# Optimization experiments

Measured on AMD Instinct MI355X. Metric: run time of the kernel, lower is better.

The kernel has to match this reference:

```python
import jax, jax.numpy as jnp
import numpy as np

FISTA_ITER = 50
LAMBDA = 0.1
POWER_ITER = 100


def power_method(W):
    # Estimates c = largest eigenvalue of W^T W (squared spectral norm).
    # Torch code uses a random init vector; we use a fixed key for determinism.
    X0 = jax.random.normal(jax.random.key(1), (1, W.shape[1]), dtype=W.dtype)

    def body(i, carry):
        X, _ = carry
        X = (X @ W.T) @ W            # [1, m]
        nm = jnp.linalg.norm(X)
        return (X / nm, nm)

    _, nm = jax.lax.fori_loop(0, POWER_ITER, body, (X0, jnp.asarray(1.0, W.dtype)))
    return nm


def soft_threshold(X, lam):
    return jnp.sign(X) * jax.nn.relu(jnp.abs(X) - lam)


def fista(Y, W, lam, iters):
    c = power_method(W)
    eta = 1.0 / c
    Gamma0 = soft_threshold(Y @ (eta * W), lam)   # [B, m]
    Y_norm = jnp.linalg.norm(Y)
    t0 = jnp.asarray(1.0, Y.dtype)

    def step(carry, _):
        Gamma, Z, t = carry
        residual = Z @ W.T - Y                                   # [B, n]
        Gamma_new = soft_threshold(Z - eta * (residual @ W), lam / c)
        t_new = (1.0 + jnp.sqrt(1.0 + 4.0 * t ** 2)) / 2.0
        Z_new = Gamma_new + (t - 1.0) / t_new * (Gamma_new - Gamma)
        nrm = jnp.linalg.norm(residual) / Y_norm
        return (Gamma_new, Z_new, t_new), nrm

    (Gamma, _, _), norms = jax.lax.scan(step, (Gamma0, Gamma0, t0), None, length=iters)
    return Gamma, norms


def setup_inputs() -> dict:
    key = jax.random.key(0)
    k1, k2 = jax.random.split(key)
    Y = jax.random.normal(k1, (8192, 784), dtype=jnp.float32)
    W = jax.random.normal(k2, (784, 2048), dtype=jnp.float32)
    W = W / jnp.linalg.norm(W, axis=0, keepdims=True)  # NormDict
    return {"Y": Y, "W": W}


def reference(Y, W):
    Gamma, norms = fista(Y, W, LAMBDA, FISTA_ITER)
    X = Gamma @ W.T                  # reconstruction [B, 784]
    return (X, Gamma, norms)
```

## Files before the change

kernel.cpp:

```cpp
#include <hip/hip_runtime.h>
#include <math.h>

#define B_DIM   8192
#define N_DIM   784
#define NPAD    800
#define NROWS_W 896
#define M_DIM   2048
#define XSZ     (B_DIM*N_DIM)
#define GSZ     (B_DIM*M_DIM)
#define NITER   50
#define PITER   100

typedef __attribute__((ext_vector_type(8))) short short8;
typedef __attribute__((ext_vector_type(4))) float floatx4;

__device__ __forceinline__ void async_ld16(const unsigned short* g, unsigned short* l){
  __builtin_amdgcn_global_load_lds(
      (const __attribute__((address_space(1))) unsigned int*)g,
      (__attribute__((address_space(3))) unsigned int*)l,
      16, 0, 0);
}

__device__ __forceinline__ unsigned rotl32(unsigned x, int d){ return (x<<d)|(x>>(32-d)); }

__device__ void threefry2x32(unsigned& v0, unsigned& v1){
  const unsigned ks0=0u, ks1=1u, ks2=0x1BD11BDBu;
  unsigned x0=v0+ks0, x1=v1+ks1;
#define RND(R) { x0+=x1; x1=rotl32(x1,R); x1^=x0; }
  RND(13) RND(15) RND(26) RND(6)
  x0+=ks1; x1+=ks2+1u;
  RND(17) RND(29) RND(16) RND(24)
  x0+=ks2; x1+=ks0+2u;
  RND(13) RND(15) RND(26) RND(6)
  x0+=ks0; x1+=ks1+3u;
  RND(17) RND(29) RND(16) RND(24)
  x0+=ks1; x1+=ks2+4u;
  RND(13) RND(15) RND(26) RND(6)
  x0+=ks2; x1+=ks0+5u;
#undef RND
  v0=x0; v1=x1;
}

__device__ float erfinv_f(float x){
  float w = -logf((1.0f-x)*(1.0f+x));
  float p;
  if (w < 5.0f){
    w -= 2.5f;
    p = 2.81022636e-08f;
    p = fmaf(p,w, 3.43273939e-07f);
    p = fmaf(p,w,-3.5233877e-06f);
    p = fmaf(p,w,-4.39150654e-06f);
    p = fmaf(p,w, 0.00021858087f);
    p = fmaf(p,w,-0.00125372503f);
    p = fmaf(p,w,-0.00417768164f);
    p = fmaf(p,w, 0.246640727f);
    p = fmaf(p,w, 1.50140941f);
  } else {
    w = sqrtf(w) - 3.0f;
    p = -0.000200214257f;
    p = fmaf(p,w, 0.000100950558f);
    p = fmaf(p,w, 0.00134934322f);
    p = fmaf(p,w,-0.00367342844f);
    p = fmaf(p,w, 0.00573950773f);
    p = fmaf(p,w,-0.0076224613f);
    p = fmaf(p,w, 0.00943887047f);
    p = fmaf(p,w, 1.00167406f);
    p = fmaf(p,w, 2.83297682f);
  }
  return p*x;
}

__device__ float bits_to_normal(unsigned b){
  unsigned fb = (b>>9) | 0x3f800000u;
  float u01 = __uint_as_float(fb) - 1.0f;
  const float lo = -0.99999994f;
  float u = u01*(1.0f - lo) + lo;
  u = fmaxf(lo, u);
  return 1.41421356237f * erfinv_f(u);
}

__global__ void setup_kernel(float* __restrict__ xbuf0, float* __restrict__ accs){
  int i = threadIdx.x;
  if (i < 64) accs[i] = 0.0f;
  unsigned v0 = (unsigned)i, v1 = (unsigned)(1024+i);
  threefry2x32(v0, v1);
  xbuf0[i]        = bits_to_normal(v0);
  xbuf0[1024 + i] = bits_to_normal(v1);
}

__device__ __forceinline__ unsigned short f2bf(float f){
  unsigned u = __float_as_uint(f);
  unsigned r = (u + 0x7fffu + ((u>>16)&1u)) >> 16;
  return (unsigned short)r;
}
__device__ __forceinline__ unsigned pack2(float a, float b){
  return (unsigned)f2bf(a) | ((unsigned)f2bf(b) << 16);
}
__device__ __forceinline__ float bf2f(unsigned short s){
  return __uint_as_float(((unsigned)s) << 16);
}

__global__ void conv_w(const float* __restrict__ W, unsigned short* __restrict__ Wbf){
  int i4 = (blockIdx.x*256 + threadIdx.x)*4;
  int row = i4 >> 11;
  uint2 p = make_uint2(0,0);
  if (row < N_DIM){
    float4 v = *(const float4*)(W + (size_t)row*M_DIM + (i4 & 2047));
    p.x = pack2(v.x, v.y); p.y = pack2(v.z, v.w);
  }
  *(uint2*)(Wbf + i4) = p;
}

__global__ void conv_y(const float* __restrict__ Y, unsigned short* __restrict__ Ybf){
  int row = blockIdx.x;
  int c4 = threadIdx.x*4;
  if (c4 >= NPAD) return;
  uint2 p = make_uint2(0,0);
  if (c4 < N_DIM){
    float4 v = *(const float4*)(Y + (size_t)row*N_DIM + c4);
    p.x = pack2(v.x, v.y); p.y = pack2(v.z, v.w);
  }
  *(uint2*)(Ybf + (size_t)row*NPAD + c4) = p;
}

__global__ void transpose_w(const float* __restrict__ W, unsigned short* __restrict__ WTbf){
  __shared__ float tile[32][33];
  int k0 = blockIdx.x*32;
  int j0 = blockIdx.y*32;
  int tx = threadIdx.x & 31, ty = threadIdx.x >> 5;
#pragma unroll
  for (int i=0;i<4;i++){
    int j = j0 + ty + 8*i;
    float v = (j < N_DIM) ? W[(size_t)j*M_DIM + k0 + tx] : 0.0f;
    tile[tx][ty+8*i] = v;
  }
  __syncthreads();
#pragma unroll
  for (int i=0;i<4;i++){
    int k = k0 + ty + 8*i;
    WTbf[(size_t)k*NPAD + j0 + tx] = f2bf(tile[ty+8*i][tx]);
  }
}

__global__ __launch_bounds__(256)
void compute_q(const float* __restrict__ W, float* __restrict__ Q){
  __shared__ float As2[16][132];
  __shared__ float Bs2[16][132];
  const int t = threadIdx.x;
  const int a0 = blockIdx.x*128, b0 = blockIdx.y*128;
  const int ty = t>>4, tx = t&15;
  float acc[8][8];
#pragma unroll
  for (int i=0;i<8;i++)
#pragma unroll
    for (int j=0;j<8;j++) acc[i][j]=0.0f;

  for (int j0=0; j0<N_DIM; j0+=16){
#pragma unroll
    for (int h=0; h<8; ++h){
      int idx = h*256 + t;
      int r = idx>>7, c = idx&127;
      As2[r][c] = W[(size_t)(j0+r)*M_DIM + a0 + c];
      Bs2[r][c] = W[(size_t)(j0+r)*M_DIM + b0 + c];
    }
    __syncthreads();
#pragma unroll
    for (int kk=0; kk<16; ++kk){
      float a[8], b[8];
#pragma unroll
      for (int i=0;i<8;i++) a[i] = As2[kk][ty*8+i];
#pragma unroll
      for (int j=0;j<8;j++) b[j] = Bs2[kk][tx*8+j];
#pragma unroll
      for (int i=0;i<8;i++)
#pragma unroll
        for (int j=0;j<8;j++) acc[i][j] = fmaf(a[i], b[j], acc[i][j]);
    }
    __syncthreads();
  }
#pragma unroll
  for (int i=0;i<8;i++){
    int a = a0 + ty*8 + i;
#pragma unroll
    for (int j=0;j<8;j++) Q[(size_t)a*M_DIM + b0 + tx*8 + j] = acc[i][j];
  }
}

__global__ void sumsq_kernel(const float* __restrict__ v, int n, float* __restrict__ acc){
  __shared__ float red[256];
  int t = threadIdx.x;
  float s = 0.0f;
  for (int i = blockIdx.x*256 + t; i < n; i += gridDim.x*256){ float x = v[i]; s = fmaf(x,x,s); }
  red[t] = s; __syncthreads();
  for (int off=128; off>0; off>>=1){ if (t<off) red[t]+=red[t+off]; __syncthreads(); }
  if (t==0) atomicAdd(acc, red[0]);
}

__global__ void pm_q(const float* __restrict__ x, const float* __restrict__ Q,
                     float* __restrict__ xout){
  __shared__ float red[256];
  int t = threadIdx.x;
  float s = 0.0f;
  for (int k=t; k<M_DIM; k+=256){ float v = x[k]; s = fmaf(v,v,s); }
  red[t]=s; __syncthreads();
  for (int off=128; off>0; off>>=1){ if (t<off) red[t]+=red[t+off]; __syncthreads(); }
  float inv = 1.0f/sqrtf(red[0]);
  int wave = t>>6, lane = t&63;
  int j = blockIdx.x*4 + wave;
  const float* Qr = Q + (size_t)j*M_DIM;
  float acc = 0.0f;
  for (int k=lane; k<M_DIM; k+=64) acc = fmaf(x[k], Qr[k], acc);
  for (int off=32; off>0; off>>=1) acc += __shfl_down(acc, off);
  if (lane==0) xout[j] = acc * inv;
}

__global__ void finish_power(const float* __restrict__ xfin, const float* __restrict__ accs,
                             float* __restrict__ params){
  __shared__ float red[256];
  int t = threadIdx.x;
  float s = 0.0f;
  for (int k=t; k<M_DIM; k+=256){ float v = xfin[k]; s = fmaf(v,v,s); }
  red[t]=s; __syncthreads();
  for (int off=128; off>0; off>>=1){ if (t<off) red[t]+=red[t+off]; __syncthreads(); }
  if (t==0){
    float c = sqrtf(red[0]);
    params[0] = c;
    params[1] = 1.0f/c;
    params[2] = 0.1f/c;
    params[3] = sqrtf(accs[0]);
  }
}

__device__ __forceinline__ float softthr(float v, float th){
  float a = fmaxf(fabsf(v) - th, 0.0f);
  return copysignf(a, v);
}

template<int MODE>
__global__ __launch_bounds__(256)
void mfma_nt(const unsigned short* __restrict__ Abf,
             const unsigned short* __restrict__ Bbf,
             const float* __restrict__ Wf,
             const float* __restrict__ Y,
             unsigned short* __restrict__ Rbf,
             float* __restrict__ X,
             float* __restrict__ nacc){
  __shared__ float4 smem4[1024];
  unsigned short* As = (unsigned short*)smem4;
  unsigned short* Bs = As + 64*32;
  float* fbuf = (float*)smem4;

  const int t    = threadIdx.x;
  const int m0   = blockIdx.x*64, n0 = blockIdx.y*128;
  const int wave = t>>6, lane = t&63;
  const int wm2  = wave>>1, wn2 = wave&1;
  const int quad = lane>>4, l15 = lane&15;
  const int lrow = lane>>2;
  const int lk   = (lane&3)*8;
  const int sr   = t>>1;
  const int skq  = (t&1)*16;

  floatx4 acc[2][4];
#pragma unroll
  for (int i=0;i<2;i++)
#pragma unroll
    for (int j=0;j<4;j++) acc[i][j] = (floatx4)(0.0f);

  for (int k0=0; k0<M_DIM; k0+=32){
    async_ld16(Abf + (size_t)(m0 + wave*16 + lrow)*M_DIM + k0 + lk, &As[wave*512]);
    if (MODE==0){
#pragma unroll
      for (int c=0; c<2; ++c){
        int chunk = wave*2 + c;
        async_ld16(Bbf + (size_t)(n0 + chunk*16 + lrow)*M_DIM + k0 + lk, &Bs[chunk*512]);
      }
    } else {
      int j = n0 + sr;
      uint4 p0 = make_uint4(0,0,0,0), p1 = make_uint4(0,0,0,0);
      if (j < N_DIM){
        const float* bp = Wf + (size_t)j*M_DIM + k0 + skq;
        float4 v0 = *(const float4*)(bp+0);
        float4 v1 = *(const float4*)(bp+4);
        float4 v2 = *(const float4*)(bp+8);
        float4 v3 = *(const float4*)(bp+12);
        p0.x=pack2(v0.x,v0.y); p0.y=pack2(v0.z,v0.w); p0.z=pack2(v1.x,v1.y); p0.w=pack2(v1.z,v1.w);
        p1.x=pack2(v2.x,v2.y); p1.y=pack2(v2.z,v2.w); p1.z=pack2(v3.x,v3.y); p1.w=pack2(v3.z,v3.w);
      }
      *(uint4*)&Bs[sr*32 + skq]     = p0;
      *(uint4*)&Bs[sr*32 + skq + 8] = p1;
    }
    __syncthreads();
    short8 af[2], bfr[4];
#pragma unroll
    for (int ti=0; ti<2; ++ti)
      af[ti] = *(const short8*)&As[(wm2*32 + ti*16 + l15)*32 + quad*8];
#pragma unroll
    for (int tj=0; tj<4; ++tj)
      bfr[tj] = *(const short8*)&Bs[(wn2*64 + tj*16 + l15)*32 + quad*8];
#pragma unroll
    for (int ti=0; ti<2; ++ti)
#pragma unroll
      for (int tj=0; tj<4; ++tj)
        acc[ti][tj] = __builtin_amdgcn_mfma_f32_16x16x32_bf16(af[ti], bfr[tj], acc[ti][tj], 0, 0, 0);
    __syncthreads();
  }

  float ss = 0.0f;
#pragma unroll
  for (int c=0; c<2; ++c){
    if (wn2 == c){
#pragma unroll
      for (int ti=0; ti<2; ++ti)
#pragma unroll
        for (int tj=0; tj<4; ++tj)
#pragma unroll
          for (int r=0; r<4; ++r)
            fbuf[(wm2*32 + ti*16 + quad*4 + r)*64 + tj*16 + l15] = acc[ti][tj][r];
    }
    __syncthreads();
#pragma unroll
    for (int k=0; k<4; ++k){
      int row = k*16 + (t>>4);
      int col = (t&15)*4;
      int m = m0 + row;
      int n = n0 + c*64 + col;
      float4 v = *(const float4*)&fbuf[row*64 + col];
      if (MODE==0){
        if (n < N_DIM){
          float4 yv = *(const float4*)(Y + (size_t)m*N_DIM + n);
          float r0 = v.x - yv.x, r1 = v.y - yv.y, r2 = v.z - yv.z, r3 = v.w - yv.w;
          uint2 p; p.x = pack2(r0, r1); p.y = pack2(r2, r3);
          *(uint2*)(Rbf + (size_t)m*NPAD + n) = p;
          ss = fmaf(r0,r0, fmaf(r1,r1, fmaf(r2,r2, fmaf(r3,r3, ss))));
        } else if (n < NPAD){
          *(uint2*)(Rbf + (size_t)m*NPAD + n) = make_uint2(0,0);
        }
      } else {
        if (n < N_DIM) *(float4*)(X + (size_t)m*N_DIM + n) = v;
      }
    }
    __syncthreads();
  }

  if (MODE==0){
    for (int off=32; off>0; off>>=1) ss += __shfl_down(ss, off);
    if (lane==0) atomicAdd(nacc, ss);
  }
}

template<int MODE>
__global__ __launch_bounds__(256)
void mfma_nn(const unsigned short* __restrict__ Abf,
             const unsigned short* __restrict__ WTbf,
             float* __restrict__ Gamma,
             unsigned short* __restrict__ Zhi,
             unsigned short* __restrict__ Zlo,
             const float* __restrict__ params,
             float mu){
  __shared__ float4 smem4[1024];
  unsigned short* As = (unsigned short*)smem4;
  unsigned short* Bs = As + 128*32;
  float* fbuf = (float*)smem4;

  const int t    = threadIdx.x;
  const int m0   = blockIdx.x*128, n0 = blockIdx.y*128;
  const int wave = t>>6, lane = t&63;
  const int wm   = wave>>1, wn = wave&1;
  const int quad = lane>>4, l15 = lane&15;
  const int ch0  = wave*2;
  const int lrow = lane>>2;
  const int lk   = (lane&3)*8;

  floatx4 acc[4][4];
#pragma unroll
  for (int i=0;i<4;i++)
#pragma unroll
    for (int j=0;j<4;j++) acc[i][j] = (floatx4)(0.0f);

  for (int k0=0; k0<NPAD; k0+=32){
#pragma unroll
    for (int c=0; c<2; ++c){
      int chunk = ch0 + c;
      async_ld16(Abf  + (size_t)(m0 + chunk*16 + lrow)*NPAD + k0 + lk, &As[chunk*512]);
      async_ld16(WTbf + (size_t)(n0 + chunk*16 + lrow)*NPAD + k0 + lk, &Bs[chunk*512]);
    }
    __syncthreads();
    short8 af[4], bfr[4];
#pragma unroll
    for (int ti=0; ti<4; ++ti)
      af[ti] = *(const short8*)&As[(wm*64 + ti*16 + l15)*32 + quad*8];
#pragma unroll
    for (int tj=0; tj<4; ++tj)
      bfr[tj] = *(const short8*)&Bs[(wn*64 + tj*16 + l15)*32 + quad*8];
#pragma unroll
    for (int ti=0; ti<4; ++ti)
#pragma unroll
      for (int tj=0; tj<4; ++tj)
        acc[ti][tj] = __builtin_amdgcn_mfma_f32_16x16x32_bf16(af[ti], bfr[tj], acc[ti][tj], 0, 0, 0);
    __syncthreads();
  }

  const float eta  = params[1];
  const float lamc = params[2];

#pragma unroll
  for (int c=0; c<4; ++c){
    if (wn == (c>>1)){
      int tjb = (c&1)*2;
#pragma unroll
      for (int ti=0; ti<4; ++ti)
#pragma unroll
        for (int u=0; u<2; ++u)
#pragma unroll
          for (int r=0; r<4; ++r)
            fbuf[(wm*64 + ti*16 + quad*4 + r)*32 + u*16 + l15] = acc[ti][tjb+u][r];
    }
    __syncthreads();
#pragma unroll
    for (int k=0; k<4; ++k){
      int row = k*32 + (t>>3);
      int col = (t&7)*4;
      int m = m0 + row;
      int n = n0 + c*32 + col;
      size_t idx = (size_t)m*M_DIM + n;
      float4 g4 = *(const float4*)&fbuf[row*32 + col];
      float gr[4] = {g4.x, g4.y, g4.z, g4.w};
      float go4[4];
      if (MODE!=0){
        uint2 ph = *(const uint2*)(Zhi + idx);
        uint2 pl = *(const uint2*)(Zlo + idx);
        unsigned short h[4] = {(unsigned short)(ph.x&0xffff),(unsigned short)(ph.x>>16),
                               (unsigned short)(ph.y&0xffff),(unsigned short)(ph.y>>16)};
        unsigned short l[4] = {(unsigned short)(pl.x&0xffff),(unsigned short)(pl.x>>16),
                               (unsigned short)(pl.y&0xffff),(unsigned short)(pl.y>>16)};
        float4 gov = *(const float4*)(Gamma + idx);
        go4[0]=gov.x; go4[1]=gov.y; go4[2]=gov.z; go4[3]=gov.w;
#pragma unroll
        for (int e=0;e<4;e++){
          float zv = bf2f(h[e]) + bf2f(l[e]);
          gr[e] = softthr(zv - eta*gr[e], lamc);
        }
      } else {
#pragma unroll
        for (int e=0;e<4;e++) gr[e] = softthr(eta*gr[e], 0.1f);
      }
      *(float4*)(Gamma + idx) = make_float4(gr[0],gr[1],gr[2],gr[3]);
      if (MODE==1){
        float zn[4];
#pragma unroll
        for (int e=0;e<4;e++) zn[e] = gr[e] + mu*(gr[e] - go4[e]);
        unsigned short h0=f2bf(zn[0]), h1=f2bf(zn[1]), h2=f2bf(zn[2]), h3=f2bf(zn[3]);
        uint2 ph; ph.x = (unsigned)h0 | ((unsigned)h1<<16); ph.y = (unsigned)h2 | ((unsigned)h3<<16);
        uint2 pl; pl.x = pack2(zn[0]-bf2f(h0), zn[1]-bf2f(h1));
                  pl.y = pack2(zn[2]-bf2f(h2), zn[3]-bf2f(h3));
        *(uint2*)(Zhi + idx) = ph;
        *(uint2*)(Zlo + idx) = pl;
      } else if (MODE==0){
        unsigned short h0=f2bf(gr[0]), h1=f2bf(gr[1]), h2=f2bf(gr[2]), h3=f2bf(gr[3]);
        uint2 ph; ph.x = (unsigned)h0 | ((unsigned)h1<<16); ph.y = (unsigned)h2 | ((unsigned)h3<<16);
        uint2 pl; pl.x = pack2(gr[0]-bf2f(h0), gr[1]-bf2f(h1));
                  pl.y = pack2(gr[2]-bf2f(h2), gr[3]-bf2f(h3));
        *(uint2*)(Zhi + idx) = ph;
        *(uint2*)(Zlo + idx) = pl;
      } else {
        uint2 ph; ph.x = pack2(gr[0], gr[1]); ph.y = pack2(gr[2], gr[3]);
        *(uint2*)(Zhi + idx) = ph;
      }
    }
    __syncthreads();
  }
}

__global__ void norms_finalize(const float* __restrict__ nacc, const float* __restrict__ params,
                               float* __restrict__ out){
  int i = threadIdx.x;
  if (i < NITER) out[i] = sqrtf(nacc[i]) / params[3];
}

extern "C" void kernel_launch(void* const* d_in, const int* in_sizes, int n_in,
                              void* d_out, int out_size, void* d_ws, size_t ws_size,
                              hipStream_t stream){
  const float* Y  = (const float*)d_in[0];
  const float* W  = (const float*)d_in[1];
  float* out      = (float*)d_out;
  float* X        = out;
  float* Gamma    = out + XSZ;
  float* norms    = out + XSZ + GSZ;

  unsigned short* Zhi = (unsigned short*)d_ws;
  unsigned short* Zlo = Zhi + (size_t)B_DIM*M_DIM;

  unsigned short* Wbf  = (unsigned short*)out;
  unsigned short* WTbf = Wbf + (size_t)NROWS_W*M_DIM;
  unsigned short* Rbf  = WTbf + (size_t)M_DIM*NPAD;
  float* Q      = (float*)Rbf;
  float* fsc    = (float*)(Rbf + (size_t)M_DIM*M_DIM*2);
  float* xb0    = fsc;
  float* xb1    = xb0 + M_DIM;
  float* params = xb1 + M_DIM;
  float* accs   = params + 8;

  setup_kernel<<<dim3(1), dim3(1024), 0, stream>>>(xb0, accs);
  sumsq_kernel<<<dim3(512), dim3(256), 0, stream>>>(Y, XSZ, accs);
  conv_w      <<<dim3(1792), dim3(256), 0, stream>>>(W, Wbf);
  transpose_w <<<dim3(64,25), dim3(256), 0, stream>>>(W, WTbf);

  compute_q<<<dim3(16,16), dim3(256), 0, stream>>>(W, Q);
  float* xa = xb0; float* xc = xb1;
  for (int it=0; it<PITER; ++it){
    pm_q<<<dim3(512), dim3(256), 0, stream>>>(xa, Q, xc);
    float* tmp = xa; xa = xc; xc = tmp;
  }
  finish_power<<<dim3(1), dim3(256), 0, stream>>>(xa, accs, params);

  conv_y<<<dim3(B_DIM), dim3(256), 0, stream>>>(Y, Rbf);

  mfma_nn<0><<<dim3(64,16), dim3(256), 0, stream>>>(Rbf, WTbf, Gamma, Zhi, Zlo, params, 0.0f);

  float tcur = 1.0f;
  for (int it=0; it<NITER; ++it){
    mfma_nt<0><<<dim3(128,7), dim3(256), 0, stream>>>(Zhi, Wbf, nullptr, Y, Rbf, nullptr, accs + 1 + it);
    float tsq = tcur*tcur;
    float tn  = (1.0f + sqrtf(1.0f + 4.0f*tsq)) / 2.0f;
    float mu  = (tcur - 1.0f) / tn;
    tcur = tn;
    if (it < NITER-1)
      mfma_nn<1><<<dim3(64,16), dim3(256), 0, stream>>>(Rbf, WTbf, Gamma, Zhi, Zlo, params, mu);
    else
      mfma_nn<2><<<dim3(64,16), dim3(256), 0, stream>>>(Rbf, WTbf, Gamma, Zhi, Zlo, params, mu);
  }

  norms_finalize<<<dim3(1), dim3(64), 0, stream>>>(accs + 1, params, norms);

  mfma_nt<1><<<dim3(128,7), dim3(256), 0, stream>>>(Zhi, nullptr, W, nullptr, nullptr, X, nullptr);
}
```

Baseline: 9.635 ms.

## Widen GEMM tiles to 256 columns with XCD-aware block mapping

Both MFMA GEMM kernels now compute 256-column output tiles per block (doubling accumulators per wave) and use a 1D grid of 512 blocks whose index is remapped so consecutive blocks land on the same XCD group and share A rows. Scratch buffers (Wbf, WTbf, Rbf, Q) move from the output buffer into the workspace, and the final reconstruction reuses the padded bf16 W copy instead of converting fp32 W inline. This aims to cut redundant operand loads and improve L2 locality, at the cost of higher register pressure, more LDS, and fewer blocks than CUs for wave-level parallelism.

After: 9.278 ms. -3.7%, faster.

```diff
diff --git a/kernel.cpp b/kernel.cpp
--- a/kernel.cpp
+++ b/kernel.cpp
@@ -4,7 +4,7 @@
 #define B_DIM   8192
 #define N_DIM   784
 #define NPAD    800
-#define NROWS_W 896
+#define NROWS_W 1024
 #define M_DIM   2048
 #define XSZ     (B_DIM*N_DIM)
 #define GSZ     (B_DIM*M_DIM)
@@ -240,82 +240,68 @@
 __global__ __launch_bounds__(256)
 void mfma_nt(const unsigned short* __restrict__ Abf,
              const unsigned short* __restrict__ Bbf,
-             const float* __restrict__ Wf,
              const float* __restrict__ Y,
              unsigned short* __restrict__ Rbf,
              float* __restrict__ X,
              float* __restrict__ nacc){
-  __shared__ float4 smem4[1024];
+  __shared__ float4 smem4[1280];
   unsigned short* As = (unsigned short*)smem4;
   unsigned short* Bs = As + 64*32;
   float* fbuf = (float*)smem4;
 
+  const int bid = blockIdx.x;
+  const int g8  = bid & 7, w = bid >> 3;
+  const int m0  = (g8*16 + (w>>2))*64;
+  const int n0  = (w & 3)*256;
+
   const int t    = threadIdx.x;
-  const int m0   = blockIdx.x*64, n0 = blockIdx.y*128;
   const int wave = t>>6, lane = t&63;
   const int wm2  = wave>>1, wn2 = wave&1;
   const int quad = lane>>4, l15 = lane&15;
   const int lrow = lane>>2;
   const int lk   = (lane&3)*8;
-  const int sr   = t>>1;
-  const int skq  = (t&1)*16;
-
-  floatx4 acc[2][4];
+
+  floatx4 acc[2][8];
 #pragma unroll
   for (int i=0;i<2;i++)
 #pragma unroll
-    for (int j=0;j<4;j++) acc[i][j] = (floatx4)(0.0f);
+    for (int j=0;j<8;j++) acc[i][j] = (floatx4)(0.0f);
 
   for (int k0=0; k0<M_DIM; k0+=32){
     async_ld16(Abf + (size_t)(m0 + wave*16 + lrow)*M_DIM + k0 + lk, &As[wave*512]);
-    if (MODE==0){
-#pragma unroll
-      for (int c=0; c<2; ++c){
-        int chunk = wave*2 + c;
-        async_ld16(Bbf + (size_t)(n0 + chunk*16 + lrow)*M_DIM + k0 + lk, &Bs[chunk*512]);
-      }
-    } else {
-      int j = n0 + sr;
-      uint4 p0 = make_uint4(0,0,0,0), p1 = make_uint4(0,0,0,0);
-      if (j < N_DIM){
-        const float* bp = Wf + (size_t)j*M_DIM + k0 + skq;
-        float4 v0 = *(const float4*)(bp+0);
-        float4 v1 = *(const float4*)(bp+4);
-        float4 v2 = *(const float4*)(bp+8);
-        float4 v3 = *(const float4*)(bp+12);
-        p0.x=pack2(v0.x,v0.y); p0.y=pack2(v0.z,v0.w); p0.z=pack2(v1.x,v1.y); p0.w=pack2(v1.z,v1.w);
-        p1.x=pack2(v2.x,v2.y); p1.y=pack2(v2.z,v2.w); p1.z=pack2(v3.x,v3.y); p1.w=pack2(v3.z,v3.w);
-      }
-      *(uint4*)&Bs[sr*32 + skq]     = p0;
-      *(uint4*)&Bs[sr*32 + skq + 8] = p1;
-    }
-    __syncthreads();
-    short8 af[2], bfr[4];
+#pragma unroll
+    for (int c=0; c<4; ++c){
+      int chunk = wave*4 + c;
+      async_ld16(Bbf + (size_t)(n0 + chunk*16 + lrow)*M_DIM + k0 + lk, &Bs[chunk*512]);
+    }
+    __syncthreads();
+    short8 af[2], bfr[8];
 #pragma unroll
     for (int ti=0; ti<2; ++ti)
       af[ti] = *(const short8*)&As[(wm2*32 + ti*16 + l15)*32 + quad*8];
 #pragma unroll
-    for (int tj=0; tj<4; ++tj)
-      bfr[tj] = *(const short8*)&Bs[(wn2*64 + tj*16 + l15)*32 + quad*8];
+    for (int tj=0; tj<8; ++tj)
+      bfr[tj] = *(const short8*)&Bs[(wn2*128 + tj*16 + l15)*32 + quad*8];
 #pragma unroll
     for (int ti=0; ti<2; ++ti)
 #pragma unroll
-      for (int tj=0; tj<4; ++tj)
+      for (int tj=0; tj<8; ++tj)
         acc[ti][tj] = __builtin_amdgcn_mfma_f32_16x16x32_bf16(af[ti], bfr[tj], acc[ti][tj], 0, 0, 0);
     __syncthreads();
   }
 
   float ss = 0.0f;
 #pragma unroll
-  for (int c=0; c<2; ++c){
-    if (wn2 == c){
+  for (int c=0; c<4; ++c){
+    if (wn2 == (c>>1)){
+      int tb = (c&1)*4;
 #pragma unroll
       for (int ti=0; ti<2; ++ti)
 #pragma unroll
-        for (int tj=0; tj<4; ++tj)
+        for (int u=0; u<4; ++u)
 #pragma unroll
           for (int r=0; r<4; ++r)
-            fbuf[(wm2*32 + ti*16 + quad*4 + r)*64 + tj*16 + l15] = acc[ti][tj][r];
+            fbuf[(wm2*32 + ti*16 + quad*4 + r)*64 + u*16 + l15] = acc[ti][tb+u][r];
     }
     __syncthreads();
 #pragma unroll
@@ -357,45 +343,52 @@
              unsigned short* __restrict__ Zlo,
              const float* __restrict__ params,
              float mu){
-  __shared__ float4 smem4[1024];
+  __shared__ float4 smem4[1536];
   unsigned short* As = (unsigned short*)smem4;
   unsigned short* Bs = As + 128*32;
   float* fbuf = (float*)smem4;
 
+  const int bid = blockIdx.x;
+  const int g8  = bid & 7, w = bid >> 3;
+  const int m0  = (g8*8 + (w>>3))*128;
+  const int n0  = (w & 7)*256;
+
   const int t    = threadIdx.x;
-  const int m0   = blockIdx.x*128, n0 = blockIdx.y*128;
   const int wave = t>>6, lane = t&63;
   const int wm   = wave>>1, wn = wave&1;
   const int quad = lane>>4, l15 = lane&15;
-  const int ch0  = wave*2;
   const int lrow = lane>>2;
   const int lk   = (lane&3)*8;
 
-  floatx4 acc[4][4];
+  floatx4 acc[4][8];
 #pragma unroll
   for (int i=0;i<4;i++)
 #pragma unroll
-    for (int j=0;j<4;j++) acc[i][j] = (floatx4)(0.0f);
+    for (int j=0;j<8;j++) acc[i][j] = (floatx4)(0.0f);
 
   for (int k0=0; k0<NPAD; k0+=32){
 #pragma unroll
     for (int c=0; c<2; ++c){
-      int chunk = ch0 + c;
-      async_ld16(Abf  + (size_t)(m0 + chunk*16 + lrow)*NPAD + k0 + lk, &As[chunk*512]);
+      int chunk = wave*2 + c;
+      async_ld16(Abf + (size_t)(m0 + chunk*16 + lrow)*NPAD + k0 + lk, &As[chunk*512]);
+    }
+#pragma unroll
+    for (int c=0; c<4; ++c){
+      int chunk = wave*4 + c;
       async_ld16(WTbf + (size_t)(n0 + chunk*16 + lrow)*NPAD + k0 + lk, &Bs[chunk*512]);
     }
     __syncthreads();
-    short8 af[4], bfr[4];
+    short8 af[4], bfr[8];
 #pragma unroll
     for (int ti=0; ti<4; ++ti)
       af[ti] = *(const short8*)&As[(wm*64 + ti*16 + l15)*32 + quad*8];
 #pragma unroll
-    for (int tj=0; tj<4; ++tj)
-      bfr[tj] = *(const short8*)&Bs[(wn*64 + tj*16 + l15)*32 + quad*8];
+    for (int tj=0; tj<8; ++tj)
+      bfr[tj] = *(const short8*)&Bs[(wn*128 + tj*16 + l15)*32 + quad*8];
 #pragma unroll
     for (int ti=0; ti<4; ++ti)
 #pragma unroll
-      for (int tj=0; tj<4; ++tj)
+      for (int tj=0; tj<8; ++tj)
         acc[ti][tj] = __builtin_amdgcn_mfma_f32_16x16x32_bf16(af[ti], bfr[tj], acc[ti][tj], 0, 0, 0);
     __syncthreads();
   }
@@ -404,16 +397,16 @@
   const float lamc = params[2];
 
 #pragma unroll
-  for (int c=0; c<4; ++c){
-    if (wn == (c>>1)){
-      int tjb = (c&1)*2;
+  for (int c=0; c<8; ++c){
+    if (wn == (c>>2)){
+      int tb = (c&3)*2;
 #pragma unroll
       for (int ti=0; ti<4; ++ti)
 #pragma unroll
         for (int u=0; u<2; ++u)
 #pragma unroll
           for (int r=0; r<4; ++r)
-            fbuf[(wm*64 + ti*16 + quad*4 + r)*32 + u*16 + l15] = acc[ti][tjb+u][r];
+            fbuf[(wm*64 + ti*16 + quad*4 + r)*32 + u*16 + l15] = acc[ti][tb+u][r];
     }
     __syncthreads();
 #pragma unroll
@@ -487,23 +480,22 @@
   float* Gamma    = out + XSZ;
   float* norms    = out + XSZ + GSZ;
 
-  unsigned short* Zhi = (unsigned short*)d_ws;
-  unsigned short* Zlo = Zhi + (size_t)B_DIM*M_DIM;
-
-  unsigned short* Wbf  = (unsigned short*)out;
-  unsigned short* WTbf = Wbf + (size_t)NROWS_W*M_DIM;
-  unsigned short* Rbf  = WTbf + (size_t)M_DIM*NPAD;
-  float* Q      = (float*)Rbf;
-  float* fsc    = (float*)(Rbf + (size_t)M_DIM*M_DIM*2);
-  float* xb0    = fsc;
+  unsigned short* Zhi  = (unsigned short*)d_ws;
+  unsigned short* Zlo  = Zhi  + (size_t)GSZ;
+  unsigned short* Rbf  = Zlo  + (size_t)GSZ;
+  unsigned short* Wbf  = Rbf  + (size_t)B_DIM*NPAD;
+  unsigned short* WTbf = Wbf  + (size_t)NROWS_W*M_DIM;
+  float* Q      = (float*)(WTbf + (size_t)M_DIM*NPAD);
+  float* xb0    = Q + (size_t)M_DIM*M_DIM;
   float* xb1    = xb0 + M_DIM;
   float* params = xb1 + M_DIM;
   float* accs   = params + 8;
 
   setup_kernel<<<dim3(1), dim3(1024), 0, stream>>>(xb0, accs);
   sumsq_kernel<<<dim3(512), dim3(256), 0, stream>>>(Y, XSZ, accs);
-  conv_w      <<<dim3(1792), dim3(256), 0, stream>>>(W, Wbf);
+  conv_w      <<<dim3(2048), dim3(256), 0, stream>>>(W, Wbf);
   transpose_w <<<dim3(64,25), dim3(256), 0, stream>>>(W, WTbf);
+  conv_y      <<<dim3(B_DIM), dim3(256), 0, stream>>>(Y, Rbf);
 
   compute_q<<<dim3(16,16), dim3(256), 0, stream>>>(W, Q);
   float* xa = xb0; float* xc = xb1;
@@ -513,24 +505,22 @@
   }
   finish_power<<<dim3(1), dim3(256), 0, stream>>>(xa, accs, params);
 
-  conv_y<<<dim3(B_DIM), dim3(256), 0, stream>>>(Y, Rbf);
-
-  mfma_nn<0><<<dim3(64,16), dim3(256), 0, stream>>>(Rbf, WTbf, Gamma, Zhi, Zlo, params, 0.0f);
+  mfma_nn<0><<<dim3(512), dim3(256), 0, stream>>>(Rbf, WTbf, Gamma, Zhi, Zlo, params, 0.0f);
 
   float tcur = 1.0f;
   for (int it=0; it<NITER; ++it){
-    mfma_nt<0><<<dim3(128,7), dim3(256), 0, stream>>>(Zhi, Wbf, nullptr, Y, Rbf, nullptr, accs + 1 + it);
+    mfma_nt<0><<<dim3(512), dim3(256), 0, stream>>>(Zhi, Wbf, Y, Rbf, nullptr, accs + 1 + it);
     float tsq = tcur*tcur;
     float tn  = (1.0f + sqrtf(1.0f + 4.0f*tsq)) / 2.0f;
     float mu  = (tcur - 1.0f) / tn;
     tcur = tn;
     if (it < NITER-1)
-      mfma_nn<1><<<dim3(64,16), dim3(256), 0, stream>>>(Rbf, WTbf, Gamma, Zhi, Zlo, params, mu);
+      mfma_nn<1><<<dim3(512), dim3(256), 0, stream>>>(Rbf, WTbf, Gamma, Zhi, Zlo, params, mu);
     else
-      mfma_nn<2><<<dim3(64,16), dim3(256), 0, stream>>>(Rbf, WTbf, Gamma, Zhi, Zlo, params, mu);
+      mfma_nn<2><<<dim3(512), dim3(256), 0, stream>>>(Rbf, WTbf, Gamma, Zhi, Zlo, params, mu);
   }
 
   norms_finalize<<<dim3(1), dim3(64), 0, stream>>>(accs + 1, params, norms);
 
-  mfma_nt<1><<<dim3(128,7), dim3(256), 0, stream>>>(Zhi, nullptr, W, nullptr, nullptr, X, nullptr);
-}
+  mfma_nt<1><<<dim3(512), dim3(256), 0, stream>>>(Zhi, Wbf, nullptr, nullptr, X, nullptr);
+}
```

## Remap GEMM blocks for XCD-aware locality and move scratch buffers to workspace

Applied to the files above, without the earlier changes.

Both MFMA kernels now launch on a 1D grid and remap block ids so that consecutive ids spread across the 8 XCDs (bid&7). Each XCD works on a contiguous band of rows, which should improve L2 reuse of the A and B tiles. Scratch buffers (bf16 W, W^T, residual, Q) move from the output region into the workspace. That lets the final reconstruction GEMM read the prebuilt bf16 W through async loads instead of converting fp32 W on the fly, and conv_y is launched earlier. The approach needs a large enough workspace, and the block-id mapping assumes the XCDs are assigned round-robin.

New measurement: 9.500 ms. Within noise of the previous version (-1.4%).

```diff
diff --git a/kernel.cpp b/kernel.cpp
--- a/kernel.cpp
+++ b/kernel.cpp
@@ -240,7 +240,6 @@
 __global__ __launch_bounds__(256)
 void mfma_nt(const unsigned short* __restrict__ Abf,
              const unsigned short* __restrict__ Bbf,
-             const float* __restrict__ Wf,
              const float* __restrict__ Y,
              unsigned short* __restrict__ Rbf,
              float* __restrict__ X,
@@ -250,15 +249,18 @@
   unsigned short* Bs = As + 64*32;
   float* fbuf = (float*)smem4;
 
+  const int bid = blockIdx.x;
+  const int g8  = bid & 7, w = bid >> 3;
+  const int mt  = w / 7, nt = w - mt*7;
+  const int m0  = (g8*16 + mt)*64;
+  const int n0  = nt*128;
+
   const int t    = threadIdx.x;
-  const int m0   = blockIdx.x*64, n0 = blockIdx.y*128;
   const int wave = t>>6, lane = t&63;
   const int wm2  = wave>>1, wn2 = wave&1;
   const int quad = lane>>4, l15 = lane&15;
   const int lrow = lane>>2;
   const int lk   = (lane&3)*8;
-  const int sr   = t>>1;
-  const int skq  = (t&1)*16;
 
   floatx4 acc[2][4];
 #pragma unroll
@@ -268,26 +270,10 @@
 
   for (int k0=0; k0<M_DIM; k0+=32){
     async_ld16(Abf + (size_t)(m0 + wave*16 + lrow)*M_DIM + k0 + lk, &As[wave*512]);
-    if (MODE==0){
-#pragma unroll
-      for (int c=0; c<2; ++c){
-        int chunk = wave*2 + c;
-        async_ld16(Bbf + (size_t)(n0 + chunk*16 + lrow)*M_DIM + k0 + lk, &Bs[chunk*512]);
-      }
-    } else {
-      int j = n0 + sr;
-      uint4 p0 = make_uint4(0,0,0,0), p1 = make_uint4(0,0,0,0);
-      if (j < N_DIM){
-        const float* bp = Wf + (size_t)j*M_DIM + k0 + skq;
-        float4 v0 = *(const float4*)(bp+0);
-        float4 v1 = *(const float4*)(bp+4);
-        float4 v2 = *(const float4*)(bp+8);
-        float4 v3 = *(const float4*)(bp+12);
-        p0.x=pack2(v0.x,v0.y); p0.y=pack2(v0.z,v0.w); p0.z=pack2(v1.x,v1.y); p0.w=pack2(v1.z,v1.w);
-        p1.x=pack2(v2.x,v2.y); p1.y=pack2(v2.z,v2.w); p1.z=pack2(v3.x,v3.y); p1.w=pack2(v3.z,v3.w);
-      }
-      *(uint4*)&Bs[sr*32 + skq]     = p0;
-      *(uint4*)&Bs[sr*32 + skq + 8] = p1;
+#pragma unroll
+    for (int c=0; c<2; ++c){
+      int chunk = wave*2 + c;
+      async_ld16(Bbf + (size_t)(n0 + chunk*16 + lrow)*M_DIM + k0 + lk, &Bs[chunk*512]);
     }
     __syncthreads();
     short8 af[2], bfr[4];
@@ -362,8 +348,12 @@
   unsigned short* Bs = As + 128*32;
   float* fbuf = (float*)smem4;
 
+  const int bid = blockIdx.x;
+  const int g8  = bid & 7, w = bid >> 3;
+  const int m0  = (g8*8 + (w>>4))*128;
+  const int n0  = (w & 15)*128;
+
   const int t    = threadIdx.x;
-  const int m0   = blockIdx.x*128, n0 = blockIdx.y*128;
   const int wave = t>>6, lane = t&63;
   const int wm   = wave>>1, wn = wave&1;
   const int quad = lane>>4, l15 = lane&15;
@@ -487,15 +477,13 @@
   float* Gamma    = out + XSZ;
   float* norms    = out + XSZ + GSZ;
 
-  unsigned short* Zhi = (unsigned short*)d_ws;
-  unsigned short* Zlo = Zhi + (size_t)B_DIM*M_DIM;
-
-  unsigned short* Wbf  = (unsigned short*)out;
-  unsigned short* WTbf = Wbf + (size_t)NROWS_W*M_DIM;
-  unsigned short* Rbf  = WTbf + (size_t)M_DIM*NPAD;
-  float* Q      = (float*)Rbf;
-  float* fsc    = (float*)(Rbf + (size_t)M_DIM*M_DIM*2);
-  float* xb0    = fsc;
+  unsigned short* Zhi  = (unsigned short*)d_ws;
+  unsigned short* Zlo  = Zhi  + (size_t)GSZ;
+  unsigned short* Rbf  = Zlo  + (size_t)GSZ;
+  unsigned short* Wbf  = Rbf  + (size_t)B_DIM*NPAD;
+  unsigned short* WTbf = Wbf  + (size_t)NROWS_W*M_DIM;
+  float* Q      = (float*)(WTbf + (size_t)M_DIM*NPAD);
+  float* xb0    = Q + (size_t)M_DIM*M_DIM;
   float* xb1    = xb0 + M_DIM;
   float* params = xb1 + M_DIM;
   float* accs   = params + 8;
@@ -504,6 +492,7 @@
   sumsq_kernel<<<dim3(512), dim3(256), 0, stream>>>(Y, XSZ, accs);
   conv_w      <<<dim3(1792), dim3(256), 0, stream>>>(W, Wbf);
   transpose_w <<<dim3(64,25), dim3(256), 0, stream>>>(W, WTbf);
+  conv_y      <<<dim3(B_DIM), dim3(256), 0, stream>>>(Y, Rbf);
 
   compute_q<<<dim3(16,16), dim3(256), 0, stream>>>(W, Q);
   float* xa = xb0; float* xc = xb1;
@@ -513,24 +502,22 @@
   }
   finish_power<<<dim3(1), dim3(256), 0, stream>>>(xa, accs, params);
 
-  conv_y<<<dim3(B_DIM), dim3(256), 0, stream>>>(Y, Rbf);
-
-  mfma_nn<0><<<dim3(64,16), dim3(256), 0, stream>>>(Rbf, WTbf, Gamma, Zhi, Zlo, params, 0.0f);
+  mfma_nn<0><<<dim3(1024), dim3(256), 0, stream>>>(Rbf, WTbf, Gamma, Zhi, Zlo, params, 0.0f);
 
   float tcur = 1.0f;
   for (int it=0; it<NITER; ++it){
-    mfma_nt<0><<<dim3(128,7), dim3(256), 0, stream>>>(Zhi, Wbf, nullptr, Y, Rbf, nullptr, accs + 1 + it);
+    mfma_nt<0><<<dim3(896), dim3(256), 0, stream>>>(Zhi, Wbf, Y, Rbf, nullptr, accs + 1 + it);
     float tsq = tcur*tcur;
     float tn  = (1.0f + sqrtf(1.0f + 4.0f*tsq)) / 2.0f;
     float mu  = (tcur - 1.0f) / tn;
     tcur = tn;
     if (it < NITER-1)
-      mfma_nn<1><<<dim3(64,16), dim3(256), 0, stream>>>(Rbf, WTbf, Gamma, Zhi, Zlo, params, mu);
+      mfma_nn<1><<<dim3(1024), dim3(256), 0, stream>>>(Rbf, WTbf, Gamma, Zhi, Zlo, params, mu);
     else
-      mfma_nn<2><<<dim3(64,16), dim3(256), 0, stream>>>(Rbf, WTbf, Gamma, Zhi, Zlo, params, mu);
+      mfma_nn<2><<<dim3(1024), dim3(256), 0, stream>>>(Rbf, WTbf, Gamma, Zhi, Zlo, params, mu);
   }
 
   norms_finalize<<<dim3(1), dim3(64), 0, stream>>>(accs + 1, params, norms);
 
-  mfma_nt<1><<<dim3(128,7), dim3(256), 0, stream>>>(Zhi, nullptr, W, nullptr, nullptr, X, nullptr);
-}
+  mfma_nt<1><<<dim3(896), dim3(256), 0, stream>>>(Zhi, Wbf, nullptr, nullptr, X, nullptr);
+}
```
